# Kernel optimization log

Hardware: AMD Instinct MI355X
Metric: run time of the kernel (lower is better)

Reference implementation:

```python
import jax, jax.numpy as jnp
import numpy as np


def setup_inputs() -> dict:
    key = jax.random.key(0)
    k1, k2, k3, k4, k5 = jax.random.split(key, 5)
    B, H, W, F = 32, 32, 32, 768
    x = jax.random.normal(k1, (B, H, W, F), dtype=jnp.float32)
    fc_w = jax.random.normal(k2, (2, F), dtype=jnp.float32) * 0.02
    fc_b = jax.random.normal(k3, (2,), dtype=jnp.float32) * 0.02
    fc_final_w = jax.random.normal(k4, (2, F), dtype=jnp.float32) * 0.02
    fc_final_b = jax.random.normal(k5, (2,), dtype=jnp.float32) * 0.02
    return {"x": x, "fc_w": fc_w, "fc_b": fc_b,
            "fc_final_w": fc_final_w, "fc_final_b": fc_final_b}


def reference(x, fc_w, fc_b, fc_final_w, fc_final_b):
    B = x.shape[0]
    F = x.shape[-1]
    tokens = x.reshape(B, -1, F)                              # [B, T, F]
    norm = jnp.linalg.norm(tokens, axis=-1, keepdims=True)
    nt = tokens / norm                                        # unit-norm tokens
    # full T x T cosine-similarity attention (faithful to original einsum)
    attention = jnp.einsum('btf,bTf->btT', nt, nt)            # [B, T, T]
    attention = jax.nn.softmax(attention, axis=-1)
    # per-token cancer probability via small linear head
    logits = jnp.einsum('btf,cf->btc', tokens, fc_w) + fc_b   # [B, T, 2]
    cancer_probs = jax.nn.softmax(logits, axis=-1)[:, :, 1]   # [B, T]
    idx = jnp.argmax(cancer_probs, axis=1)                    # [B]
    # gather the single attention row selected by argmax
    attention_idx = jnp.take_along_axis(attention, idx[:, None, None], axis=1)[:, 0, :]  # [B, T]
    attention_idx = attention_idx * cancer_probs
    attention_idx = attention_idx / attention_idx.sum(axis=-1, keepdims=True)
    x_fused = jnp.einsum('bt,btf->bf', attention_idx, tokens)  # [B, F]
    return jnp.einsum('bf,cf->bc', x_fused, fc_final_w) + fc_final_b
```

## Files before the change

### kernel.cpp

```cpp
#include <hip/hip_runtime.h>
#include <hip/hip_bf16.h>
#include <math.h>

#define BATCH 32
#define T 1024
#define F 768

__global__ __launch_bounds__(256) void k1_token_stats(
    const float* __restrict__ x, const float* __restrict__ fc_w,
    const float* __restrict__ fc_b, const float* __restrict__ fc_final_w,
    float* __restrict__ ws_p, float* __restrict__ ws_y0,
    float* __restrict__ ws_y1, float* __restrict__ ws_norm)
{
    const int wave = threadIdx.x >> 6;
    const int lane = threadIdx.x & 63;
    const int g = blockIdx.x * 4 + wave;
    const float* tok = x + (size_t)g * F;

    float asq = 0.f, a0 = 0.f, a1 = 0.f, af0 = 0.f, af1 = 0.f;
    #pragma unroll
    for (int j = 0; j < 3; ++j) {
        const int off = j * 256 + lane * 4;
        float4 v  = *(const float4*)(tok + off);
        float4 w0 = *(const float4*)(fc_w + off);
        float4 w1 = *(const float4*)(fc_w + F + off);
        float4 f0 = *(const float4*)(fc_final_w + off);
        float4 f1 = *(const float4*)(fc_final_w + F + off);
        asq += v.x*v.x  + v.y*v.y  + v.z*v.z  + v.w*v.w;
        a0  += v.x*w0.x + v.y*w0.y + v.z*w0.z + v.w*w0.w;
        a1  += v.x*w1.x + v.y*w1.y + v.z*w1.z + v.w*w1.w;
        af0 += v.x*f0.x + v.y*f0.y + v.z*f0.z + v.w*f0.w;
        af1 += v.x*f1.x + v.y*f1.y + v.z*f1.z + v.w*f1.w;
    }
    #pragma unroll
    for (int d = 32; d > 0; d >>= 1) {
        asq += __shfl_xor(asq, d);
        a0  += __shfl_xor(a0,  d);
        a1  += __shfl_xor(a1,  d);
        af0 += __shfl_xor(af0, d);
        af1 += __shfl_xor(af1, d);
    }
    if (lane == 0) {
        const float l0 = a0 + fc_b[0];
        const float l1 = a1 + fc_b[1];
        ws_p[g]    = 1.f / (1.f + expf(l0 - l1));
        ws_y0[g]   = af0;
        ws_y1[g]   = af1;
        ws_norm[g] = sqrtf(asq);
    }
}

__global__ __launch_bounds__(256) void k2_argmax(
    const float* __restrict__ ws_p, int* __restrict__ ws_idx)
{
    const int b = blockIdx.x;
    __shared__ float sv[256];
    __shared__ int   si[256];
    float best = -1e30f; int bi = 0;
    for (int t = threadIdx.x; t < T; t += 256) {
        const float p = ws_p[b * T + t];
        if (p > best) { best = p; bi = t; }
    }
    sv[threadIdx.x] = best; si[threadIdx.x] = bi;
    __syncthreads();
    for (int s = 128; s > 0; s >>= 1) {
        if (threadIdx.x < s) {
            const float o = sv[threadIdx.x + s];
            const int  oi = si[threadIdx.x + s];
            if (o > sv[threadIdx.x] ||
                (o == sv[threadIdx.x] && oi < si[threadIdx.x])) {
                sv[threadIdx.x] = o; si[threadIdx.x] = oi;
            }
        }
        __syncthreads();
    }
    if (threadIdx.x == 0) ws_idx[b] = si[0];
}

__global__ __launch_bounds__(256) void k3_attn_row(
    const float* __restrict__ x, const float* __restrict__ ws_p,
    const float* __restrict__ ws_y0, const float* __restrict__ ws_y1,
    const float* __restrict__ ws_norm, const int* __restrict__ ws_idx,
    float* __restrict__ ws_part)
{
    const int seg  = blockIdx.x;
    const int b    = blockIdx.y;
    const int wave = threadIdx.x >> 6;
    const int lane = threadIdx.x & 63;

    __shared__ float q[F];
    __shared__ float red[4][4];

    const int idx = ws_idx[b];
    const float* qg = x + ((size_t)b * T + idx) * F;
    for (int i = threadIdx.x; i < F; i += 256) q[i] = qg[i];
    __syncthreads();

    const float nq = ws_norm[b * T + idx];

    float m = -1e30f, den = 0.f, n0 = 0.f, n1 = 0.f;
    #pragma unroll
    for (int it = 0; it < 4; ++it) {
        const int t = seg * 16 + it * 4 + wave;
        const float* tok = x + ((size_t)b * T + t) * F;
        float acc = 0.f;
        #pragma unroll
        for (int j = 0; j < 3; ++j) {
            const int off = j * 256 + lane * 4;
            float4 v  = *(const float4*)(tok + off);
            float4 qq = *(const float4*)(&q[off]);
            acc += v.x*qq.x + v.y*qq.y + v.z*qq.z + v.w*qq.w;
        }
        #pragma unroll
        for (int d = 32; d > 0; d >>= 1) acc += __shfl_xor(acc, d);

        const float s  = acc / (nq * ws_norm[b * T + t]);
        const float p  = ws_p[b * T + t];
        const float y0 = ws_y0[b * T + t];
        const float y1 = ws_y1[b * T + t];
        if (s > m) {
            const float r = expf(m - s);
            den *= r; n0 *= r; n1 *= r; m = s;
        }
        const float w = expf(s - m) * p;
        den += w; n0 += w * y0; n1 += w * y1;
    }
    if (lane == 0) {
        red[wave][0] = m; red[wave][1] = den; red[wave][2] = n0; red[wave][3] = n1;
    }
    __syncthreads();
    if (threadIdx.x == 0) {
        float M = red[0][0];
        for (int w = 1; w < 4; ++w) M = fmaxf(M, red[w][0]);
        float D = 0.f, N0 = 0.f, N1 = 0.f;
        for (int w = 0; w < 4; ++w) {
            const float r = expf(red[w][0] - M);
            D += red[w][1] * r; N0 += red[w][2] * r; N1 += red[w][3] * r;
        }
        float* o = ws_part + ((size_t)b * 64 + seg) * 4;
        o[0] = M; o[1] = D; o[2] = N0; o[3] = N1;
    }
}

__global__ __launch_bounds__(64) void k4_finalize(
    const float* __restrict__ ws_part, const float* __restrict__ fc_final_b,
    float* __restrict__ out)
{
    const int b = blockIdx.x;
    const int lane = threadIdx.x;
    const float* pp = ws_part + ((size_t)b * 64 + lane) * 4;
    float m = pp[0], den = pp[1], n0 = pp[2], n1 = pp[3];
    #pragma unroll
    for (int d = 32; d > 0; d >>= 1) {
        const float om = __shfl_xor(m, d);
        const float od = __shfl_xor(den, d);
        const float o0 = __shfl_xor(n0, d);
        const float o1 = __shfl_xor(n1, d);
        const float M  = fmaxf(m, om);
        const float ra = expf(m - M), rb = expf(om - M);
        den = den * ra + od * rb;
        n0  = n0  * ra + o0 * rb;
        n1  = n1  * ra + o1 * rb;
        m = M;
    }
    if (lane == 0) {
        out[b * 2 + 0] = n0 / den + fc_final_b[0];
        out[b * 2 + 1] = n1 / den + fc_final_b[1];
    }
}

extern "C" void kernel_launch(void* const* d_in, const int* in_sizes, int n_in,
                              void* d_out, int out_size, void* d_ws, size_t ws_size,
                              hipStream_t stream) {
    const float* x          = (const float*)d_in[0];
    const float* fc_w       = (const float*)d_in[1];
    const float* fc_b       = (const float*)d_in[2];
    const float* fc_final_w = (const float*)d_in[3];
    const float* fc_final_b = (const float*)d_in[4];
    float* out = (float*)d_out;

    float* ws      = (float*)d_ws;
    float* ws_p    = ws;
    float* ws_y0   = ws + 32768;
    float* ws_y1   = ws + 65536;
    float* ws_norm = ws + 98304;
    int*   ws_idx  = (int*)(ws + 131072);
    float* ws_part = ws + 131072 + 64;

    k1_token_stats<<<dim3((BATCH * T) / 4), 256, 0, stream>>>(
        x, fc_w, fc_b, fc_final_w, ws_p, ws_y0, ws_y1, ws_norm);
    k2_argmax<<<dim3(BATCH), 256, 0, stream>>>(ws_p, ws_idx);
    k3_attn_row<<<dim3(64, BATCH), 256, 0, stream>>>(
        x, ws_p, ws_y0, ws_y1, ws_norm, ws_idx, ws_part);
    k4_finalize<<<dim3(BATCH), 64, 0, stream>>>(ws_part, fc_final_b, out);
}
```

Before: 172.9 us.

## Fuse argmax into stats kernel and drop online-softmax rescaling via atomics

```diff
diff --git a/kernel.cpp b/kernel.cpp
--- a/kernel.cpp
+++ b/kernel.cpp
@@ -6,102 +6,91 @@
 #define T 1024
 #define F 768
 
+
 __global__ __launch_bounds__(256) void k1_token_stats(
     const float* __restrict__ x, const float* __restrict__ fc_w,
     const float* __restrict__ fc_b, const float* __restrict__ fc_final_w,
-    float* __restrict__ ws_p, float* __restrict__ ws_y0,
-    float* __restrict__ ws_y1, float* __restrict__ ws_norm)
+    float4* __restrict__ stats, unsigned long long* __restrict__ best)
 {
     const int wave = threadIdx.x >> 6;
     const int lane = threadIdx.x & 63;
-    const int g = blockIdx.x * 4 + wave;
-    const float* tok = x + (size_t)g * F;
+    const int b     = blockIdx.x >> 5;
+    const int tbase = (blockIdx.x & 31) * 32;
 
-    float asq = 0.f, a0 = 0.f, a1 = 0.f, af0 = 0.f, af1 = 0.f;
+    float4 w0[3], w1[3], f0[3], f1[3];
     #pragma unroll
     for (int j = 0; j < 3; ++j) {
         const int off = j * 256 + lane * 4;
-        float4 v  = *(const float4*)(tok + off);
-        float4 w0 = *(const float4*)(fc_w + off);
-        float4 w1 = *(const float4*)(fc_w + F + off);
-        float4 f0 = *(const float4*)(fc_final_w + off);
-        float4 f1 = *(const float4*)(fc_final_w + F + off);
-        asq += v.x*v.x  + v.y*v.y  + v.z*v.z  + v.w*v.w;
-        a0  += v.x*w0.x + v.y*w0.y + v.z*w0.z + v.w*w0.w;
-        a1  += v.x*w1.x + v.y*w1.y + v.z*w1.z + v.w*w1.w;
-        af0 += v.x*f0.x + v.y*f0.y + v.z*f0.z + v.w*f0.w;
-        af1 += v.x*f1.x + v.y*f1.y + v.z*f1.z + v.w*f1.w;
+        w0[j] = *(const float4*)(fc_w + off);
+        w1[j] = *(const float4*)(fc_w + F + off);
+        f0[j] = *(const float4*)(fc_final_w + off);
+        f1[j] = *(const float4*)(fc_final_w + F + off);
     }
+    const float bias01 = fc_b[0] - fc_b[1];
+
+    float bp = -1.f; int bidx = 0;
     #pragma unroll
-    for (int d = 32; d > 0; d >>= 1) {
-        asq += __shfl_xor(asq, d);
-        a0  += __shfl_xor(a0,  d);
-        a1  += __shfl_xor(a1,  d);
-        af0 += __shfl_xor(af0, d);
-        af1 += __shfl_xor(af1, d);
+    for (int it = 0; it < 8; ++it) {
+        const int t = tbase + it * 4 + wave;
+        const float* tok = x + ((size_t)b * T + t) * F;
+        float asq = 0.f, a0 = 0.f, a1 = 0.f, af0 = 0.f, af1 = 0.f;
+        #pragma unroll
+        for (int j = 0; j < 3; ++j) {
+            float4 v = *(const float4*)(tok + j * 256 + lane * 4);
+            asq += v.x*v.x       + v.y*v.y       + v.z*v.z       + v.w*v.w;
+            a0  += v.x*w0[j].x + v.y*w0[j].y + v.z*w0[j].z + v.w*w0[j].w;
+            a1  += v.x*w1[j].x + v.y*w1[j].y + v.z*w1[j].z + v.w*w1[j].w;
+            af0 += v.x*f0[j].x + v.y*f0[j].y + v.z*f0[j].z + v.w*f0[j].w;
+            af1 += v.x*f1[j].x + v.y*f1[j].y + v.z*f1[j].z + v.w*f1[j].w;
+        }
+        #pragma unroll
+        for (int d = 32; d > 0; d >>= 1) {
+            asq += __shfl_xor(asq, d);
+            a0  += __shfl_xor(a0,  d);
+            a1  += __shfl_xor(a1,  d);
+            af0 += __shfl_xor(af0, d);
+            af1 += __shfl_xor(af1, d);
+        }
+        const float p = 1.f / (1.f + expf((a0 - a1) + bias01));
+        if (lane == 0)
+            stats[(size_t)b * T + t] = make_float4(p, af0, af1, 1.f / sqrtf(asq));
+        if (p > bp) { bp = p; bidx = t; }
     }
-    if (lane == 0) {
-        const float l0 = a0 + fc_b[0];
-        const float l1 = a1 + fc_b[1];
-        ws_p[g]    = 1.f / (1.f + expf(l0 - l1));
-        ws_y0[g]   = af0;
-        ws_y1[g]   = af1;
-        ws_norm[g] = sqrtf(asq);
+
+    __shared__ float sp[4]; __shared__ int si[4];
+    if (lane == 0) { sp[wave] = bp; si[wave] = bidx; }
+    __syncthreads();
+    if (threadIdx.x == 0) {
+        float P = sp[0]; int I = si[0];
+        for (int w = 1; w < 4; ++w)
+            if (sp[w] > P || (sp[w] == P && si[w] < I)) { P = sp[w]; I = si[w]; }
+        const unsigned long long pk =
+            ((unsigned long long)__float_as_uint(P) << 32) |
+            (unsigned long long)(0xFFFFFFFFu - (unsigned)I);
+        atomicMax(&best[b], pk);
     }
 }
 
-__global__ __launch_bounds__(256) void k2_argmax(
-    const float* __restrict__ ws_p, int* __restrict__ ws_idx)
+__global__ __launch_bounds__(256) void k3_attn_row(
+    const float* __restrict__ x, const float4* __restrict__ stats,
+    const unsigned long long* __restrict__ best, float* __restrict__ accum)
 {
-    const int b = blockIdx.x;
-    __shared__ float sv[256];
-    __shared__ int   si[256];
-    float best = -1e30f; int bi = 0;
-    for (int t = threadIdx.x; t < T; t += 256) {
-        const float p = ws_p[b * T + t];
-        if (p > best) { best = p; bi = t; }
-    }
-    sv[threadIdx.x] = best; si[threadIdx.x] = bi;
-    __syncthreads();
-    for (int s = 128; s > 0; s >>= 1) {
-        if (threadIdx.x < s) {
-            const float o = sv[threadIdx.x + s];
-            const int  oi = si[threadIdx.x + s];
-            if (o > sv[threadIdx.x] ||
-                (o == sv[threadIdx.x] && oi < si[threadIdx.x])) {
-                sv[threadIdx.x] = o; si[threadIdx.x] = oi;
-            }
-        }
-        __syncthreads();
-    }
-    if (threadIdx.x == 0) ws_idx[b] = si[0];
-}
-
-__global__ __launch_bounds__(256) void k3_attn_row(
-    const float* __restrict__ x, const float* __restrict__ ws_p,
-    const float* __restrict__ ws_y0, const float* __restrict__ ws_y1,
-    const float* __restrict__ ws_norm, const int* __restrict__ ws_idx,
-    float* __restrict__ ws_part)
-{
-    const int seg  = blockIdx.x;
-    const int b    = blockIdx.y;
+    const int b     = blockIdx.x >> 3;
+    const int tbase = (blockIdx.x & 7) * 128;
     const int wave = threadIdx.x >> 6;
     const int lane = threadIdx.x & 63;
 
+    const int idx = (int)(0xFFFFFFFFu - (unsigned)(best[b] & 0xFFFFFFFFull));
+
     __shared__ float q[F];
-    __shared__ float red[4][4];
-
-    const int idx = ws_idx[b];
+    const float4 qs = stats[(size_t)b * T + idx];
     const float* qg = x + ((size_t)b * T + idx) * F;
-    for (int i = threadIdx.x; i < F; i += 256) q[i] = qg[i];
+    for (int i = threadIdx.x; i < F; i += 256) q[i] = qg[i] * qs.w;
     __syncthreads();
 
-    const float nq = ws_norm[b * T + idx];
-
-    float m = -1e30f, den = 0.f, n0 = 0.f, n1 = 0.f;
-    #pragma unroll
-    for (int it = 0; it < 4; ++it) {
-        const int t = seg * 16 + it * 4 + wave;
+    float den = 0.f, n0 = 0.f, n1 = 0.f;
+    for (int it = 0; it < 32; ++it) {
+        const int t = tbase + it * 4 + wave;
         const float* tok = x + ((size_t)b * T + t) * F;
         float acc = 0.f;
         #pragma unroll
@@ -113,59 +102,32 @@
         }
         #pragma unroll
         for (int d = 32; d > 0; d >>= 1) acc += __shfl_xor(acc, d);
+        const float4 st = stats[(size_t)b * T + t];
+        const float w = expf(acc * st.w) * st.x;
+        den += w; n0 += w * st.y; n1 += w * st.z;
+    }
 
-        const float s  = acc / (nq * ws_norm[b * T + t]);
-        const float p  = ws_p[b * T + t];
-        const float y0 = ws_y0[b * T + t];
-        const float y1 = ws_y1[b * T + t];
-        if (s > m) {
-            const float r = expf(m - s);
-            den *= r; n0 *= r; n1 *= r; m = s;
-        }
-        const float w = expf(s - m) * p;
-        den += w; n0 += w * y0; n1 += w * y1;
-    }
-    if (lane == 0) {
-        red[wave][0] = m; red[wave][1] = den; red[wave][2] = n0; red[wave][3] = n1;
-    }
+    __shared__ float red[4][3];
+    if (lane == 0) { red[wave][0] = den; red[wave][1] = n0; red[wave][2] = n1; }
     __syncthreads();
     if (threadIdx.x == 0) {
-        float M = red[0][0];
-        for (int w = 1; w < 4; ++w) M = fmaxf(M, red[w][0]);
         float D = 0.f, N0 = 0.f, N1 = 0.f;
-        for (int w = 0; w < 4; ++w) {
-            const float r = expf(red[w][0] - M);
-            D += red[w][1] * r; N0 += red[w][2] * r; N1 += red[w][3] * r;
-        }
-        float* o = ws_part + ((size_t)b * 64 + seg) * 4;
-        o[0] = M; o[1] = D; o[2] = N0; o[3] = N1;
+        for (int w = 0; w < 4; ++w) { D += red[w][0]; N0 += red[w][1]; N1 += red[w][2]; }
+        atomicAdd(&accum[b * 4 + 0], D);
+        atomicAdd(&accum[b * 4 + 1], N0);
+        atomicAdd(&accum[b * 4 + 2], N1);
     }
 }
 
 __global__ __launch_bounds__(64) void k4_finalize(
-    const float* __restrict__ ws_part, const float* __restrict__ fc_final_b,
+    const float* __restrict__ accum, const float* __restrict__ fc_final_b,
     float* __restrict__ out)
 {
-    const int b = blockIdx.x;
-    const int lane = threadIdx.x;
-    const float* pp = ws_part + ((size_t)b * 64 + lane) * 4;
-    float m = pp[0], den = pp[1], n0 = pp[2], n1 = pp[3];
-    #pragma unroll
-    for (int d = 32; d > 0; d >>= 1) {
-        const float om = __shfl_xor(m, d);
-        const float od = __shfl_xor(den, d);
-        const float o0 = __shfl_xor(n0, d);
-        const float o1 = __shfl_xor(n1, d);
-        const float M  = fmaxf(m, om);
-        const float ra = expf(m - M), rb = expf(om - M);
-        den = den * ra + od * rb;
-        n0  = n0  * ra + o0 * rb;
-        n1  = n1  * ra + o1 * rb;
-        m = M;
-    }
-    if (lane == 0) {
-        out[b * 2 + 0] = n0 / den + fc_final_b[0];
-        out[b * 2 + 1] = n1 / den + fc_final_b[1];
+    const int b = threadIdx.x;
+    if (b < BATCH) {
+        const float D = accum[b * 4], N0 = accum[b * 4 + 1], N1 = accum[b * 4 + 2];
+        out[b * 2 + 0] = N0 / D + fc_final_b[0];
+        out[b * 2 + 1] = N1 / D + fc_final_b[1];
     }
 }
 
@@ -179,18 +141,14 @@
     const float* fc_final_b = (const float*)d_in[4];
     float* out = (float*)d_out;
 
-    float* ws      = (float*)d_ws;
-    float* ws_p    = ws;
-    float* ws_y0   = ws + 32768;
-    float* ws_y1   = ws + 65536;
-    float* ws_norm = ws + 98304;
-    int*   ws_idx  = (int*)(ws + 131072);
-    float* ws_part = ws + 131072 + 64;
+    char* ws = (char*)d_ws;
+    unsigned long long* best = (unsigned long long*)ws;
+    float*  accum = (float*)(ws + 256);
+    float4* stats = (float4*)(ws + 4096);
 
-    k1_token_stats<<<dim3((BATCH * T) / 4), 256, 0, stream>>>(
-        x, fc_w, fc_b, fc_final_w, ws_p, ws_y0, ws_y1, ws_norm);
-    k2_argmax<<<dim3(BATCH), 256, 0, stream>>>(ws_p, ws_idx);
-    k3_attn_row<<<dim3(64, BATCH), 256, 0, stream>>>(
-        x, ws_p, ws_y0, ws_y1, ws_norm, ws_idx, ws_part);
-    k4_finalize<<<dim3(BATCH), 64, 0, stream>>>(ws_part, fc_final_b, out);
+    hipMemsetAsync(ws, 0, 768, stream);
+    k1_token_stats<<<dim3(BATCH * 32), 256, 0, stream>>>(
+        x, fc_w, fc_b, fc_final_w, stats, best);
+    k3_attn_row<<<dim3(BATCH * 8), 256, 0, stream>>>(x, stats, best, accum);
+    k4_finalize<<<dim3(1), 64, 0, stream>>>(accum, fc_final_b, out);
 }
```

Measured after the change: 178.5 us. +3.2%, slower.
